# Optimization experiments

Hardware: AMD Instinct MI355X
Metric: run time of the kernel (lower is better)

## Reference

```python
import jax, jax.numpy as jnp
import numpy as np

N, E, IN_CH, C, H, L, NCLS = 4096, 131072, 512, 256, 4, 3, 2
DH = C // H  # MHA head dim


def _ln(x, g, b, eps=1e-5):
    mu = x.mean(-1, keepdims=True)
    var = ((x - mu) ** 2).mean(-1, keepdims=True)
    return (x - mu) * jax.lax.rsqrt(var + eps) * g + b


def _gelu(x):
    return jax.nn.gelu(x, approximate=False)  # torch nn.GELU default (erf)


def _gatv2(x, src, dst, wl, wr, att, b):
    # x: [N,C]; wl/wr: [H*C, C]; att: [H,C]; b: [C]
    xl = (x @ wl.T).reshape(N, H, C)  # source transform
    e = jax.nn.leaky_relu(xl[src] + (x @ wr.T).reshape(N, H, C)[dst], 0.2)  # [Et,H,C]
    score = jnp.einsum('ehc,hc->eh', e, att)  # [Et,H]
    m = jax.ops.segment_max(score, dst, num_segments=N)
    ex = jnp.exp(score - m[dst])
    denom = jax.ops.segment_sum(ex, dst, num_segments=N)
    alpha = ex / denom[dst]  # segment softmax over incoming edges
    out = jax.ops.segment_sum(alpha[:, :, None] * xl[src], dst, num_segments=N)
    return out.mean(axis=1) + b  # concat=False -> head mean


def _mha(x, in_w, in_b, out_w, out_b):
    qkv = x @ in_w.T + in_b  # [N,3C]
    q, k, v = [t.reshape(N, H, DH) for t in jnp.split(qkv, 3, axis=-1)]
    scores = jnp.einsum('nhd,mhd->hnm', q, k) / np.sqrt(DH)
    probs = jax.nn.softmax(scores, axis=-1)
    o = jnp.einsum('hnm,mhd->nhd', probs, v).reshape(N, C)
    return o @ out_w.T + out_b


def setup_inputs() -> dict:
    key = jax.random.key(0)
    ks = iter(jax.random.split(key, 64))
    s = lambda shape, sc=0.05: jax.random.normal(next(ks), shape, jnp.float32) * sc
    d = {
        'x': jax.random.normal(next(ks), (N, IN_CH), jnp.float32),
        'edge_index': jax.random.randint(next(ks), (2, E), 0, N, jnp.int32),
        'in_w': s((C, IN_CH)), 'in_b': jnp.zeros((C,), jnp.float32),
        'gat_wl': s((L, H * C, C)), 'gat_wr': s((L, H * C, C)),
        'gat_att': s((L, H, C)), 'gat_b': jnp.zeros((L, C), jnp.float32),
        'mha_in_w': s((L, 3 * C, C)), 'mha_in_b': jnp.zeros((L, 3 * C), jnp.float32),
        'mha_out_w': s((L, C, C)), 'mha_out_b': jnp.zeros((L, C), jnp.float32),
        'ln1_g': jnp.ones((L, C), jnp.float32), 'ln1_b': jnp.zeros((L, C), jnp.float32),
        'ln2_g': jnp.ones((L, C), jnp.float32), 'ln2_b': jnp.zeros((L, C), jnp.float32),
        'ln3_g': jnp.ones((L, C), jnp.float32), 'ln3_b': jnp.zeros((L, C), jnp.float32),
        'ffn_w1': s((L, 2 * C, C)), 'ffn_b1': jnp.zeros((L, 2 * C), jnp.float32),
        'ffn_w2': s((L, C, 2 * C)), 'ffn_b2': jnp.zeros((L, C), jnp.float32),
        'out_w1': s((C, C)), 'out_b1': jnp.zeros((C,), jnp.float32),
        'out_w2': s((NCLS, C)), 'out_b2': jnp.zeros((NCLS,), jnp.float32),
    }
    return d


def reference(x, edge_index, in_w, in_b, gat_wl, gat_wr, gat_att, gat_b,
              mha_in_w, mha_in_b, mha_out_w, mha_out_b,
              ln1_g, ln1_b, ln2_g, ln2_b, ln3_g, ln3_b,
              ffn_w1, ffn_b1, ffn_w2, ffn_b2,
              out_w1, out_b1, out_w2, out_b2):
    # add self loops (PyG GATv2Conv default)
    loop = jnp.arange(N, dtype=edge_index.dtype)
    src = jnp.concatenate([edge_index[0], loop])
    dst = jnp.concatenate([edge_index[1], loop])

    h = x @ in_w.T + in_b  # input_proj
    for l in range(L):
        local = _gatv2(h, src, dst, gat_wl[l], gat_wr[l], gat_att[l], gat_b[l])
        h = _ln(h + local, ln1_g[l], ln1_b[l])
        attn = _mha(h, mha_in_w[l], mha_in_b[l], mha_out_w[l], mha_out_b[l])
        h = _ln(h + attn, ln2_g[l], ln2_b[l])
        ffn = _gelu(h @ ffn_w1[l].T + ffn_b1[l]) @ ffn_w2[l].T + ffn_b2[l]
        h = _ln(h + ffn, ln3_g[l], ln3_b[l])
    h = _gelu(h @ out_w1.T + out_b1)
    return h @ out_w2.T + out_b2
```

## Files before the change

kernel.cpp:

```cpp
#include <hip/hip_runtime.h>
#include <cstdint>
#include <cstddef>

typedef unsigned short u16;
typedef __bf16 bf16x8 __attribute__((ext_vector_type(8)));
typedef float f32x4 __attribute__((ext_vector_type(4)));

constexpr int kN  = 4096;
constexpr int kE  = 131072;
constexpr int kET = kE + kN;
constexpr int kIn = 512;
constexpr int kC  = 256;
constexpr int kL  = 3;

constexpr int NSPLIT = 4;
constexpr int KSPAN  = kN / NSPLIT;
constexpr int NSTEP  = KSPAN / 64;

__device__ __forceinline__ u16 f2bf(float f) {
    unsigned u = __builtin_bit_cast(unsigned, f);
    u += 0x7fffu + ((u >> 16) & 1u);
    return (u16)(u >> 16);
}
__device__ __forceinline__ float bf2f(u16 s) {
    unsigned u = ((unsigned)s) << 16;
    return __builtin_bit_cast(float, u);
}
__device__ __forceinline__ float gelu_erf(float x) {
    return 0.5f * x * (1.f + erff(x * 0.70710678118654752f));
}
__device__ __forceinline__ void gload_lds16(const u16* gsrc, u16* ldst) {
    __builtin_amdgcn_global_load_lds(
        (const __attribute__((address_space(1))) unsigned int*)gsrc,
        (__attribute__((address_space(3))) unsigned int*)ldst, 16, 0, 0);
}
__device__ __forceinline__ float dpp_ror_add16(float x) {
    int t;
    t = __builtin_amdgcn_update_dpp(0, __builtin_bit_cast(int, x), 0x121, 0xf, 0xf, true);
    x += __builtin_bit_cast(float, t);
    t = __builtin_amdgcn_update_dpp(0, __builtin_bit_cast(int, x), 0x122, 0xf, 0xf, true);
    x += __builtin_bit_cast(float, t);
    t = __builtin_amdgcn_update_dpp(0, __builtin_bit_cast(int, x), 0x124, 0xf, 0xf, true);
    x += __builtin_bit_cast(float, t);
    t = __builtin_amdgcn_update_dpp(0, __builtin_bit_cast(int, x), 0x128, 0xf, 0xf, true);
    x += __builtin_bit_cast(float, t);
    return x;
}
__device__ __forceinline__ void unpack8(uint4 u, float* x) {
    x[0] = __builtin_bit_cast(float, u.x << 16);
    x[1] = __builtin_bit_cast(float, u.x & 0xffff0000u);
    x[2] = __builtin_bit_cast(float, u.y << 16);
    x[3] = __builtin_bit_cast(float, u.y & 0xffff0000u);
    x[4] = __builtin_bit_cast(float, u.z << 16);
    x[5] = __builtin_bit_cast(float, u.z & 0xffff0000u);
    x[6] = __builtin_bit_cast(float, u.w << 16);
    x[7] = __builtin_bit_cast(float, u.w & 0xffff0000u);
}

__global__ void cast_f2b(const float* __restrict__ src, u16* __restrict__ dst, int n4) {
    int i = blockIdx.x * blockDim.x + threadIdx.x;
    if (i >= n4) return;
    float4 v = ((const float4*)src)[i];
    ushort4 o;
    o.x = f2bf(v.x); o.y = f2bf(v.y); o.z = f2bf(v.z); o.w = f2bf(v.w);
    ((ushort4*)dst)[i] = o;
}

__global__ void csr_count(const int* __restrict__ ei, int* __restrict__ cnt) {
    int e = blockIdx.x * 256 + threadIdx.x;
    if (e >= kET) return;
    int d = (e < kE) ? ei[kE + e] : (e - kE);
    atomicAdd(cnt + d, 1);
}

__global__ __launch_bounds__(1024) void csr_scan(int* __restrict__ cnt_cur, int* __restrict__ off) {
    __shared__ int lds[1024];
    int t = threadIdx.x;
    int c[4], s = 0;
#pragma unroll
    for (int j = 0; j < 4; ++j) { c[j] = cnt_cur[t * 4 + j]; s += c[j]; }
    lds[t] = s;
    __syncthreads();
    for (int d = 1; d < 1024; d <<= 1) {
        int v = (t >= d) ? lds[t - d] : 0;
        __syncthreads();
        lds[t] += v;
        __syncthreads();
    }
    int excl = lds[t] - s;
#pragma unroll
    for (int j = 0; j < 4; ++j) { off[t * 4 + j] = excl; cnt_cur[t * 4 + j] = excl; excl += c[j]; }
    if (t == 1023) off[4096] = excl;
}

__global__ void csr_scatter(const int* __restrict__ ei, int* __restrict__ cur, int* __restrict__ csrc) {
    int e = blockIdx.x * 256 + threadIdx.x;
    if (e >= kET) return;
    int s, d;
    if (e < kE) { s = ei[e]; d = ei[kE + e]; } else { s = d = e - kE; }
    int pos = atomicAdd(cur + d, 1);
    csrc[pos] = s;
}

template <int BM, int K, int ACT, int WF32, int WBF16>
__global__ __launch_bounds__(256) void gemm_st(
    const u16* __restrict__ A, const u16* __restrict__ W,
    const float* __restrict__ bias, float* __restrict__ Cf,
    u16* __restrict__ Cb, int N) {
    constexpr int BK = 32;
    constexpr int NK = K / BK;
    constexpr int MF = BM / 32;
    int tid = threadIdx.x;
    int w = tid >> 6, lane = tid & 63;
    int wr = w >> 1, wc = w & 1;
    int g = lane >> 4, r = lane & 15;
    int bm = blockIdx.y * BM;
    int bn = blockIdx.x * 64;
    __shared__ __align__(16) u16 Ab[2][BM * BK];
    __shared__ __align__(16) u16 Bb[2][64 * BK];
    int srow = w * 16 + (lane >> 2);
    int scol = (lane & 3) * 8;
    auto stage = [&](int buf, int k0) {
#pragma unroll
        for (int i = 0; i < BM / 64; ++i)
            gload_lds16(A + (size_t)(bm + i * 64 + srow) * K + k0 + scol,
                        &Ab[buf][(i * 64 + w * 16) * BK]);
        gload_lds16(W + (size_t)(bn + srow) * K + k0 + scol, &Bb[buf][w * 16 * BK]);
    };
    f32x4 acc[MF][2] = {};
    stage(0, 0);
    __syncthreads();
    for (int st = 0; st < NK; ++st) {
        int cur = st & 1;
        if (st + 1 < NK) stage(cur ^ 1, (st + 1) * BK);
        const u16* Al = &Ab[cur][0];
        const u16* Bl = &Bb[cur][0];
        bf16x8 bf[2];
#pragma unroll
        for (int u = 0; u < 2; ++u)
            bf[u] = *(const bf16x8*)(Bl + (wc * 32 + u * 16 + r) * BK + g * 8);
#pragma unroll
        for (int t = 0; t < MF; ++t) {
            bf16x8 af = *(const bf16x8*)(Al + (wr * (BM / 2) + t * 16 + r) * BK + g * 8);
#pragma unroll
            for (int u = 0; u < 2; ++u)
                acc[t][u] = __builtin_amdgcn_mfma_f32_16x16x32_bf16(af, bf[u], acc[t][u], 0, 0, 0);
        }
        __syncthreads();
    }
    int r0 = bm + wr * (BM / 2) + g * 4;
    int c0 = bn + wc * 32 + r;
#pragma unroll
    for (int t = 0; t < MF; ++t)
#pragma unroll
        for (int u = 0; u < 2; ++u)
#pragma unroll
            for (int e = 0; e < 4; ++e) {
                int row = r0 + t * 16 + e, col = c0 + u * 16;
                float v = acc[t][u][e];
                if (bias) v += bias[col];
                if (ACT == 1) v = gelu_erf(v);
                if (WF32) Cf[(size_t)row * N + col] = v;
                if (WBF16) Cb[(size_t)row * N + col] = f2bf(v);
            }
}

__global__ __launch_bounds__(256) void ln_res(
    const float* hin, const float* add,
    const float* __restrict__ g, const float* __restrict__ b,
    float* hout, u16* __restrict__ hbf) {
    int row = blockIdx.x * 4 + (threadIdx.x >> 6);
    int lane = threadIdx.x & 63;
    const float4 x4 = *(const float4*)(hin + (size_t)row * kC + lane * 4);
    const float4 a4 = *(const float4*)(add + (size_t)row * kC + lane * 4);
    float v[4] = {x4.x + a4.x, x4.y + a4.y, x4.z + a4.z, x4.w + a4.w};
    float s = v[0] + v[1] + v[2] + v[3];
    for (int d = 1; d < 64; d <<= 1) s += __shfl_xor(s, d);
    float mu = s * (1.f / kC);
    float q = 0.f;
#pragma unroll
    for (int j = 0; j < 4; ++j) { float d = v[j] - mu; q += d * d; }
    for (int d = 1; d < 64; d <<= 1) q += __shfl_xor(q, d);
    float rstd = rsqrtf(q * (1.f / kC) + 1e-5f);
    const float4 g4 = *(const float4*)(g + lane * 4);
    const float4 b4 = *(const float4*)(b + lane * 4);
    float y0 = (v[0] - mu) * rstd * g4.x + b4.x;
    float y1 = (v[1] - mu) * rstd * g4.y + b4.y;
    float y2 = (v[2] - mu) * rstd * g4.z + b4.z;
    float y3 = (v[3] - mu) * rstd * g4.w + b4.w;
    *(float4*)(hout + (size_t)row * kC + lane * 4) = make_float4(y0, y1, y2, y3);
    ushort4 o; o.x = f2bf(y0); o.y = f2bf(y1); o.z = f2bf(y2); o.w = f2bf(y3);
    *(ushort4*)(hbf + (size_t)row * kC + lane * 4) = o;
}

__global__ __launch_bounds__(256) void gat_agg(
    const u16* __restrict__ xg,
    const float* __restrict__ att, const float* __restrict__ gb,
    const int* __restrict__ off, const int* __restrict__ srcs,
    const float* __restrict__ lng, const float* __restrict__ lnb,
    float* __restrict__ h, u16* __restrict__ hbf) {
    int n = blockIdx.x;
    int w = threadIdx.x >> 6, lane = threadIdx.x & 63;
    int q = lane >> 4, t = lane & 15;
    int cb = w * 256 + t * 16;

    uint4 xru0 = *(const uint4*)(xg + (size_t)n * 2048 + 1024 + cb);
    uint4 xru1 = *(const uint4*)(xg + (size_t)n * 2048 + 1024 + cb + 8);
    float xrv[16];
    unpack8(xru0, xrv); unpack8(xru1, xrv + 8);
    float att6[16], att4[16];
#pragma unroll
    for (int j = 0; j < 16; j += 4) {
        float4 a4 = *(const float4*)(att + cb + j);
        att6[j] = 0.6f * a4.x; att6[j + 1] = 0.6f * a4.y;
        att6[j + 2] = 0.6f * a4.z; att6[j + 3] = 0.6f * a4.w;
        att4[j] = (2.f / 3.f) * att6[j]; att4[j + 1] = (2.f / 3.f) * att6[j + 1];
        att4[j + 2] = (2.f / 3.f) * att6[j + 2]; att4[j + 3] = (2.f / 3.f) * att6[j + 3];
    }

    int i0 = off[n], i1 = off[n + 1];
    float m = -1e30f, ls = 0.f;
    float acc[16] = {};
    int i = i0 + q;
    uint4 p0a, p1a, p0b, p1b;
    if (i < i1) {
        int s = srcs[i];
        p0a = *(const uint4*)(xg + (size_t)s * 2048 + cb);
        p1a = *(const uint4*)(xg + (size_t)s * 2048 + cb + 8);
    }
    if (i + 4 < i1) {
        int s = srcs[i + 4];
        p0b = *(const uint4*)(xg + (size_t)s * 2048 + cb);
        p1b = *(const uint4*)(xg + (size_t)s * 2048 + cb + 8);
    }
    while (i < i1) {
        uint4 c0 = p0a, c1 = p1a;
        p0a = p0b; p1a = p1b;
        if (i + 8 < i1) {
            int s2 = srcs[i + 8];
            p0b = *(const uint4*)(xg + (size_t)s2 * 2048 + cb);
            p1b = *(const uint4*)(xg + (size_t)s2 * 2048 + cb + 8);
        }
        float x[16];
        unpack8(c0, x); unpack8(c1, x + 8);
        float p = 0.f;
#pragma unroll
        for (int j = 0; j < 16; ++j) {
            float e = x[j] + xrv[j];
            p = fmaf(att6[j], e, p);
            p = fmaf(att4[j], __builtin_fabsf(e), p);
        }
        p = dpp_ror_add16(p);
        if (p > m) {
            float c = __expf(m - p);
            ls = ls * c + 1.f;
#pragma unroll
            for (int j = 0; j < 16; ++j) acc[j] = acc[j] * c + x[j];
            m = p;
        } else {
            float pw = __expf(p - m);
            ls += pw;
#pragma unroll
            for (int j = 0; j < 16; ++j) acc[j] = fmaf(pw, x[j], acc[j]);
        }
        i += 4;
    }
    float mm = fmaxf(m, __shfl_xor(m, 16));
    mm = fmaxf(mm, __shfl_xor(mm, 32));
    float c = __expf(m - mm);
    ls *= c;
    ls += __shfl_xor(ls, 16);
    ls += __shfl_xor(ls, 32);
#pragma unroll
    for (int j = 0; j < 16; ++j) {
        float a = acc[j] * c;
        a += __shfl_xor(a, 16);
        a += __shfl_xor(a, 32);
        acc[j] = a;
    }
    float inv = 1.f / ls;
    __shared__ float red[4][256];
    __shared__ float rs[8];
    if (q == 0) {
#pragma unroll
        for (int j = 0; j < 16; ++j) red[w][t * 16 + j] = acc[j] * inv;
    }
    __syncthreads();
    int cc = threadIdx.x;
    float vsum = 0.25f * (red[0][cc] + red[1][cc] + red[2][cc] + red[3][cc]) + gb[cc];
    float v = h[(size_t)n * kC + cc] + vsum;
    float s1 = v, s2 = v * v;
    for (int d = 1; d < 64; d <<= 1) { s1 += __shfl_xor(s1, d); s2 += __shfl_xor(s2, d); }
    if (lane == 0) { rs[w] = s1; rs[4 + w] = s2; }
    __syncthreads();
    s1 = rs[0] + rs[1] + rs[2] + rs[3];
    s2 = rs[4] + rs[5] + rs[6] + rs[7];
    float mu = s1 * (1.f / kC);
    float rstd = rsqrtf(s2 * (1.f / kC) - mu * mu + 1e-5f);
    float y = (v - mu) * rstd * lng[cc] + lnb[cc];
    h[(size_t)n * kC + cc] = y;
    hbf[(size_t)n * kC + cc] = f2bf(y);
}

__global__ __launch_bounds__(256) void qkv_repack(
    const u16* __restrict__ qkvb, u16* __restrict__ Qb, u16* __restrict__ Kb,
    u16* __restrict__ VTb) {
    int h = blockIdx.y;
    int n0 = blockIdx.x * 64;
    int t = threadIdx.x;
    int nr = t >> 2, cb = (t & 3) * 16;
    const u16* src = qkvb + (size_t)(n0 + nr) * 768 + h * 64 + cb;
    u16* qd = Qb + ((size_t)h * kN + n0 + nr) * 64 + cb;
    u16* kd = Kb + ((size_t)h * kN + n0 + nr) * 64 + cb;
    __shared__ u16 lds[64][72];
    constexpr float QS = 0.125f * 1.4426950408889634f;
#pragma unroll
    for (int j = 0; j < 16; j += 4) {
        ushort4 q4 = *(const ushort4*)(src + j);
        ushort4 k4 = *(const ushort4*)(src + 256 + j);
        ushort4 v4 = *(const ushort4*)(src + 512 + j);
        ushort4 qo;
        qo.x = f2bf(bf2f(q4.x) * QS); qo.y = f2bf(bf2f(q4.y) * QS);
        qo.z = f2bf(bf2f(q4.z) * QS); qo.w = f2bf(bf2f(q4.w) * QS);
        *(ushort4*)(qd + j) = qo;
        *(ushort4*)(kd + j) = k4;
        *(ushort4*)(&lds[nr][cb + j]) = v4;
    }
    __syncthreads();
    int d = t >> 2, nb = (t & 3) * 16;
    u16* vd = VTb + ((size_t)h * 64 + d) * kN + n0 + nb;
#pragma unroll
    for (int j = 0; j < 16; j += 4) {
        ushort4 vo;
        vo.x = lds[nb + j + 0][d];
        vo.y = lds[nb + j + 1][d];
        vo.z = lds[nb + j + 2][d];
        vo.w = lds[nb + j + 3][d];
        *(ushort4*)(vd + j) = vo;
    }
}

__global__ __launch_bounds__(256, 4) void mha_mfma2(
    const u16* __restrict__ Qb, const u16* __restrict__ Kb,
    const u16* __restrict__ VTb, float* __restrict__ opart, float* __restrict__ mlpart) {
    int qt = blockIdx.x, head = blockIdx.y, sp = blockIdx.z;
    int tid = threadIdx.x;
    int w = tid >> 6, lane = tid & 63;
    int g = lane >> 4, r = lane & 15;
    int q0 = qt * 64;
    const u16* Qh = Qb + ((size_t)head * kN + q0 + w * 16) * 64;
    const u16* Kh = Kb + (size_t)head * kN * 64;
    const u16* VTh = VTb + (size_t)head * 64 * kN;
    __shared__ u16 Kt[2][64 * 64];
    __shared__ u16 Vt[2][64 * 64];
    __shared__ u16 plds[4][16 * 64];
    int srow = w * 8 + (lane >> 3);
    int schunk = ((lane & 7) ^ ((lane >> 3) & 7)) * 8;
    int kbase = sp * KSPAN;

    bf16x8 qf0 = *(const bf16x8*)(Qh + r * 64 + g * 8);
    bf16x8 qf1 = *(const bf16x8*)(Qh + r * 64 + 32 + g * 8);

    auto stage = [&](int buf, int k0) {
#pragma unroll
        for (int i = 0; i < 2; ++i) {
            int row = i * 32 + srow;
            gload_lds16(Kh + (size_t)(k0 + row) * 64 + schunk, &Kt[buf][(i * 32 + w * 8) * 64]);
            gload_lds16(VTh + (size_t)row * kN + k0 + schunk, &Vt[buf][(i * 32 + w * 8) * 64]);
        }
    };

    f32x4 o[4] = {};
    float m = -3.0e38f, l = 0.f;

    stage(0, kbase);
    __syncthreads();

    int rx = r & 7;
    for (int st = 0; st < NSTEP; ++st) {
        int cur = st & 1;
        if (st + 1 < NSTEP) stage(cur ^ 1, kbase + (st + 1) * 64);
        const u16* Kl = &Kt[cur][0];
        const u16* Vl = &Vt[cur][0];
        f32x4 stt[4] = {};
#pragma unroll
        for (int t = 0; t < 4; ++t) {
            bf16x8 kf0 = *(const bf16x8*)(Kl + (16 * t + r) * 64 + ((0 + g) ^ rx) * 8);
            bf16x8 kf1 = *(const bf16x8*)(Kl + (16 * t + r) * 64 + ((4 + g) ^ rx) * 8);
            stt[t] = __builtin_amdgcn_mfma_f32_16x16x32_bf16(kf0, qf0, stt[t], 0, 0, 0);
            stt[t] = __builtin_amdgcn_mfma_f32_16x16x32_bf16(kf1, qf1, stt[t], 0, 0, 0);
        }
        float pm = stt[0][0];
#pragma unroll
        for (int t = 0; t < 4; ++t)
#pragma unroll
            for (int e = 0; e < 4; ++e) pm = fmaxf(pm, stt[t][e]);
        pm = fmaxf(pm, __shfl_xor(pm, 16));
        pm = fmaxf(pm, __shfl_xor(pm, 32));
        if (__any(pm > m)) {
            float mn = fmaxf(m, pm);
            float corr = __builtin_amdgcn_exp2f(m - mn);
            l *= corr;
            float corrq[4];
#pragma unroll
            for (int e = 0; e < 4; ++e) corrq[e] = __shfl(corr, g * 4 + e);
#pragma unroll
            for (int dt = 0; dt < 4; ++dt)
#pragma unroll
                for (int e = 0; e < 4; ++e) o[dt][e] *= corrq[e];
            m = mn;
        }
        float ls = 0.f;
        float p[4][4];
#pragma unroll
        for (int t = 0; t < 4; ++t)
#pragma unroll
            for (int e = 0; e < 4; ++e) { p[t][e] = __builtin_amdgcn_exp2f(stt[t][e] - m); ls += p[t][e]; }
        ls += __shfl_xor(ls, 16);
        ls += __shfl_xor(ls, 32);
        l += ls;
#pragma unroll
        for (int t = 0; t < 4; ++t) {
            ushort4 pk;
            pk.x = f2bf(p[t][0]); pk.y = f2bf(p[t][1]);
            pk.z = f2bf(p[t][2]); pk.w = f2bf(p[t][3]);
            int lc = (2 * t + (g >> 1)) ^ rx;
            *(ushort4*)(&plds[w][r * 64 + lc * 8 + (g & 1) * 4]) = pk;
        }
        bf16x8 pa0 = *(const bf16x8*)(&plds[w][r * 64 + (g ^ rx) * 8]);
        bf16x8 pa1 = *(const bf16x8*)(&plds[w][r * 64 + ((4 + g) ^ rx) * 8]);
#pragma unroll
        for (int dt = 0; dt < 4; ++dt) {
            bf16x8 vf0 = *(const bf16x8*)(Vl + (dt * 16 + r) * 64 + ((0 + g) ^ rx) * 8);
            bf16x8 vf1 = *(const bf16x8*)(Vl + (dt * 16 + r) * 64 + ((4 + g) ^ rx) * 8);
            o[dt] = __builtin_amdgcn_mfma_f32_16x16x32_bf16(pa0, vf0, o[dt], 0, 0, 0);
            o[dt] = __builtin_amdgcn_mfma_f32_16x16x32_bf16(pa1, vf1, o[dt], 0, 0, 0);
        }
        __syncthreads();
    }

    size_t slot = (size_t)(head * 64 + qt) * NSPLIT + sp;
    float* ob = opart + slot * 4096;
#pragma unroll
    for (int dt = 0; dt < 4; ++dt)
#pragma unroll
        for (int e = 0; e < 4; ++e)
            ob[(w * 16 + g * 4 + e) * 64 + dt * 16 + r] = o[dt][e];
    float* mlb = mlpart + slot * 128;
    if (g == 0) { mlb[w * 16 + r] = m; mlb[64 + w * 16 + r] = l; }
}

__global__ __launch_bounds__(256) void mha_merge(
    const float* __restrict__ opart, const float* __restrict__ mlpart,
    u16* __restrict__ attnb) {
    int head = blockIdx.y;
    int q = blockIdx.x * 4 + (threadIdx.x >> 6);
    int d = threadIdx.x & 63;
    int qt = q >> 6, ql = q & 63;
    size_t sb = (size_t)(head * 64 + qt) * NSPLIT;
    float ms[NSPLIT], lsv[NSPLIT];
    float mstar = -3.0e38f;
#pragma unroll
    for (int s = 0; s < NSPLIT; ++s) {
        ms[s] = mlpart[(sb + s) * 128 + ql];
        lsv[s] = mlpart[(sb + s) * 128 + 64 + ql];
        mstar = fmaxf(mstar, ms[s]);
    }
    float acc = 0.f, lsum = 0.f;
#pragma unroll
    for (int s = 0; s < NSPLIT; ++s) {
        float wgt = __builtin_amdgcn_exp2f(ms[s] - mstar);
        lsum += lsv[s] * wgt;
        acc += opart[(sb + s) * 4096 + ql * 64 + d] * wgt;
    }
    attnb[(size_t)q * kC + head * 64 + d] = f2bf(acc / lsum);
}

__global__ __launch_bounds__(256) void final_out(
    const u16* __restrict__ tbf, const float* __restrict__ w2,
    const float* __restrict__ b2, float* __restrict__ out) {
    int row = blockIdx.x * 4 + (threadIdx.x >> 6);
    int lane = threadIdx.x & 63;
    const ushort4 tv = *(const ushort4*)(tbf + (size_t)row * 256 + lane * 4);
    float t0 = bf2f(tv.x), t1 = bf2f(tv.y), t2 = bf2f(tv.z), t3 = bf2f(tv.w);
    const float4 w0 = *(const float4*)(w2 + lane * 4);
    const float4 w1 = *(const float4*)(w2 + 256 + lane * 4);
    float d0 = t0 * w0.x + t1 * w0.y + t2 * w0.z + t3 * w0.w;
    float d1 = t0 * w1.x + t1 * w1.y + t2 * w1.z + t3 * w1.w;
    for (int d = 1; d < 64; d <<= 1) { d0 += __shfl_xor(d0, d); d1 += __shfl_xor(d1, d); }
    if (lane == 0) {
        out[(size_t)row * 2 + 0] = d0 + b2[0];
        out[(size_t)row * 2 + 1] = d1 + b2[1];
    }
}

extern "C" void kernel_launch(void* const* d_in, const int* in_sizes, int n_in,
                              void* d_out, int out_size, void* d_ws, size_t ws_size,
                              hipStream_t stream) {
    (void)in_sizes; (void)n_in; (void)out_size;
    const float* x        = (const float*)d_in[0];
    const int*   ei       = (const int*)d_in[1];
    const float* in_w     = (const float*)d_in[2];
    const float* in_b     = (const float*)d_in[3];
    const float* gat_wl   = (const float*)d_in[4];
    const float* gat_wr   = (const float*)d_in[5];
    const float* gat_att  = (const float*)d_in[6];
    const float* gat_b    = (const float*)d_in[7];
    const float* mha_in_w = (const float*)d_in[8];
    const float* mha_in_b = (const float*)d_in[9];
    const float* mha_out_w= (const float*)d_in[10];
    const float* mha_out_b= (const float*)d_in[11];
    const float* ln1_g = (const float*)d_in[12];
    const float* ln1_b = (const float*)d_in[13];
    const float* ln2_g = (const float*)d_in[14];
    const float* ln2_b = (const float*)d_in[15];
    const float* ln3_g = (const float*)d_in[16];
    const float* ln3_b = (const float*)d_in[17];
    const float* ffn_w1 = (const float*)d_in[18];
    const float* ffn_b1 = (const float*)d_in[19];
    const float* ffn_w2 = (const float*)d_in[20];
    const float* ffn_b2 = (const float*)d_in[21];
    const float* out_w1 = (const float*)d_in[22];
    const float* out_b1 = (const float*)d_in[23];
    const float* out_w2 = (const float*)d_in[24];
    const float* out_b2 = (const float*)d_in[25];
    float* out = (float*)d_out;

    char* ws = (char*)d_ws;
    size_t off = 0;
    auto alloc = [&](size_t bytes) -> void* {
        void* p = (void*)(ws + off);
        off += (bytes + 255) & ~(size_t)255;
        return p;
    };
    float* h     = (float*)alloc((size_t)kN * kC * 4);
    u16*   hbf   = (u16*)  alloc((size_t)kN * kC * 2);
    float* xlb   = (float*)alloc((size_t)kN * 1024 * 4);
    float* xrb   = (float*)alloc((size_t)kN * 1024 * 4);
    float* qkv   = (float*)alloc((size_t)kN * 768 * 4);
    float* locb  = (float*)alloc((size_t)kN * kC * 4);
    u16*   attnb = (u16*)  alloc((size_t)kN * kC * 2);
    u16*   midb  = (u16*)  alloc((size_t)kN * 512 * 2);
    u16*   tbf   = (u16*)  alloc((size_t)kN * kC * 2);
    u16*   xbf   = (u16*)  alloc((size_t)kN * kIn * 2);
    u16*   wbf   = (u16*)  alloc((size_t)3342336 * 2);
    int*   coff  = (int*)  alloc((size_t)4097 * 4);
    int*   ccur  = (int*)  alloc((size_t)4096 * 4);
    int*   csrc  = (int*)  alloc((size_t)kET * 4);
    if (ws_size < off) return;

    u16* xgbf = (u16*)xlb;
    u16* Qb  = (u16*)xlb;
    u16* Kb  = Qb + (size_t)4 * kN * 64;
    u16* VTb = Kb + (size_t)4 * kN * 64;
    u16* qkvb = (u16*)qkv;
    float* opart  = xrb;
    float* mlpart = locb;

    const size_t OFF_INW  = 0;
    const size_t OFF_GAT  = 131072;
    const size_t OFF_MIN  = 1703936;
    const size_t OFF_MOUT = 2293760;
    const size_t OFF_F1   = 2490368;
    const size_t OFF_F2   = 2883584;
    const size_t OFF_O1   = 3276800;

    auto cast = [&](const float* s, u16* d, int n) {
        int n4 = n >> 2;
        cast_f2b<<<dim3((n4 + 255) / 256), dim3(256), 0, stream>>>(s, d, n4);
    };
    cast(x, xbf, kN * kIn);
    cast(in_w, wbf + OFF_INW, kC * kIn);
    for (int l = 0; l < kL; ++l) {
        cast(gat_wl + (size_t)l * 262144, wbf + OFF_GAT + (size_t)l * 524288, 262144);
        cast(gat_wr + (size_t)l * 262144, wbf + OFF_GAT + (size_t)l * 524288 + 262144, 262144);
    }
    cast(mha_in_w, wbf + OFF_MIN, kL * 768 * kC);
    cast(mha_out_w, wbf + OFF_MOUT, kL * kC * kC);
    cast(ffn_w1, wbf + OFF_F1, kL * 512 * kC);
    cast(ffn_w2, wbf + OFF_F2, kL * kC * 512);
    cast(out_w1, wbf + OFF_O1, kC * kC);

    hipMemsetAsync(ccur, 0, 4096 * 4, stream);
    csr_count<<<dim3((kET + 255) / 256), dim3(256), 0, stream>>>(ei, ccur);
    csr_scan<<<dim3(1), dim3(1024), 0, stream>>>(ccur, coff);
    csr_scatter<<<dim3((kET + 255) / 256), dim3(256), 0, stream>>>(ei, ccur, csrc);

    gemm_st<64, 512, 0, 1, 1><<<dim3(kC / 64, kN / 64), dim3(256), 0, stream>>>(
        xbf, wbf + OFF_INW, in_b, h, hbf, kC);

    for (int l = 0; l < kL; ++l) {
        gemm_st<128, 256, 0, 0, 1><<<dim3(2048 / 64, kN / 128), dim3(256), 0, stream>>>(
            hbf, wbf + OFF_GAT + (size_t)l * 524288, nullptr, nullptr, xgbf, 2048);
        gat_agg<<<dim3(kN), dim3(256), 0, stream>>>(
            xgbf, gat_att + (size_t)l * 1024, gat_b + (size_t)l * kC, coff, csrc,
            ln1_g + (size_t)l * kC, ln1_b + (size_t)l * kC, h, hbf);

        gemm_st<128, 256, 0, 0, 1><<<dim3(768 / 64, kN / 128), dim3(256), 0, stream>>>(
            hbf, wbf + OFF_MIN + (size_t)l * 768 * kC, mha_in_b + (size_t)l * 768, nullptr, qkvb, 768);
        qkv_repack<<<dim3(kN / 64, 4), dim3(256), 0, stream>>>(qkvb, Qb, Kb, VTb);
        mha_mfma2<<<dim3(kN / 64, 4, NSPLIT), dim3(256), 0, stream>>>(Qb, Kb, VTb, opart, mlpart);
        mha_merge<<<dim3(kN / 4, 4), dim3(256), 0, stream>>>(opart, mlpart, attnb);
        gemm_st<64, 256, 0, 1, 0><<<dim3(kC / 64, kN / 64), dim3(256), 0, stream>>>(
            attnb, wbf + OFF_MOUT + (size_t)l * kC * kC, mha_out_b + (size_t)l * kC, locb, nullptr, kC);
        ln_res<<<dim3(kN / 4), dim3(256), 0, stream>>>(
            h, locb, ln2_g + (size_t)l * kC, ln2_b + (size_t)l * kC, h, hbf);

        gemm_st<64, 256, 1, 0, 1><<<dim3(512 / 64, kN / 64), dim3(256), 0, stream>>>(
            hbf, wbf + OFF_F1 + (size_t)l * 512 * kC, ffn_b1 + (size_t)l * 512, nullptr, midb, 512);
        gemm_st<64, 512, 0, 1, 0><<<dim3(kC / 64, kN / 64), dim3(256), 0, stream>>>(
            midb, wbf + OFF_F2 + (size_t)l * kC * 512, ffn_b2 + (size_t)l * kC, locb, nullptr, kC);
        ln_res<<<dim3(kN / 4), dim3(256), 0, stream>>>(
            h, locb, ln3_g + (size_t)l * kC, ln3_b + (size_t)l * kC, h, hbf);
    }

    gemm_st<64, 256, 1, 0, 1><<<dim3(kC / 64, kN / 64), dim3(256), 0, stream>>>(
        hbf, wbf + OFF_O1, out_b1, nullptr, tbf, kC);
    final_out<<<dim3(kN / 4), dim3(256), 0, stream>>>(tbf, out_w2, out_b2, out);
}
```

Before: 529.0 us.

## Fuse residual LayerNorm into output GEMMs and add 128x128 tile GAT projection GEMM

```diff
diff --git a/kernel.cpp b/kernel.cpp
--- a/kernel.cpp
+++ b/kernel.cpp
@@ -165,32 +165,154 @@
             }
 }
 
-__global__ __launch_bounds__(256) void ln_res(
-    const float* hin, const float* add,
-    const float* __restrict__ g, const float* __restrict__ b,
-    float* hout, u16* __restrict__ hbf) {
-    int row = blockIdx.x * 4 + (threadIdx.x >> 6);
-    int lane = threadIdx.x & 63;
-    const float4 x4 = *(const float4*)(hin + (size_t)row * kC + lane * 4);
-    const float4 a4 = *(const float4*)(add + (size_t)row * kC + lane * 4);
-    float v[4] = {x4.x + a4.x, x4.y + a4.y, x4.z + a4.z, x4.w + a4.w};
-    float s = v[0] + v[1] + v[2] + v[3];
-    for (int d = 1; d < 64; d <<= 1) s += __shfl_xor(s, d);
-    float mu = s * (1.f / kC);
-    float q = 0.f;
-#pragma unroll
-    for (int j = 0; j < 4; ++j) { float d = v[j] - mu; q += d * d; }
-    for (int d = 1; d < 64; d <<= 1) q += __shfl_xor(q, d);
-    float rstd = rsqrtf(q * (1.f / kC) + 1e-5f);
-    const float4 g4 = *(const float4*)(g + lane * 4);
-    const float4 b4 = *(const float4*)(b + lane * 4);
-    float y0 = (v[0] - mu) * rstd * g4.x + b4.x;
-    float y1 = (v[1] - mu) * rstd * g4.y + b4.y;
-    float y2 = (v[2] - mu) * rstd * g4.z + b4.z;
-    float y3 = (v[3] - mu) * rstd * g4.w + b4.w;
-    *(float4*)(hout + (size_t)row * kC + lane * 4) = make_float4(y0, y1, y2, y3);
-    ushort4 o; o.x = f2bf(y0); o.y = f2bf(y1); o.z = f2bf(y2); o.w = f2bf(y3);
-    *(ushort4*)(hbf + (size_t)row * kC + lane * 4) = o;
+template <int K>
+__global__ __launch_bounds__(256) void gemm_128(
+    const u16* __restrict__ A, const u16* __restrict__ W,
+    u16* __restrict__ Cb, int N) {
+    constexpr int BK = 32;
+    constexpr int NK = K / BK;
+    int tid = threadIdx.x;
+    int w = tid >> 6, lane = tid & 63;
+    int wr = w >> 1, wc = w & 1;
+    int g = lane >> 4, r = lane & 15;
+    int bm = blockIdx.y * 128;
+    int bn = blockIdx.x * 128;
+    __shared__ __align__(16) u16 Ab[2][128 * BK];
+    __shared__ __align__(16) u16 Bb[2][128 * BK];
+    int srd = lane >> 2;
+    int schunk = ((lane & 3) ^ ((lane >> 3) & 3)) * 8;
+    auto stage = [&](int buf, int k0) {
+#pragma unroll
+        for (int i = 0; i < 2; ++i) {
+            int rowA = bm + i * 64 + w * 16 + srd;
+            int rowB = bn + i * 64 + w * 16 + srd;
+            gload_lds16(A + (size_t)rowA * K + k0 + schunk, &Ab[buf][(i * 64 + w * 16) * BK]);
+            gload_lds16(W + (size_t)rowB * K + k0 + schunk, &Bb[buf][(i * 64 + w * 16) * BK]);
+        }
+    };
+    f32x4 acc[4][4] = {};
+    stage(0, 0);
+    __syncthreads();
+    int rs = (r >> 1) & 3;
+    for (int st = 0; st < NK; ++st) {
+        int cur = st & 1;
+        if (st + 1 < NK) stage(cur ^ 1, (st + 1) * BK);
+        const u16* Al = &Ab[cur][0];
+        const u16* Bl = &Bb[cur][0];
+        bf16x8 bf[4];
+#pragma unroll
+        for (int u = 0; u < 4; ++u)
+            bf[u] = *(const bf16x8*)(Bl + (wc * 64 + u * 16 + r) * BK + ((g ^ rs) * 8));
+#pragma unroll
+        for (int t = 0; t < 4; ++t) {
+            bf16x8 af = *(const bf16x8*)(Al + (wr * 64 + t * 16 + r) * BK + ((g ^ rs) * 8));
+#pragma unroll
+            for (int u = 0; u < 4; ++u)
+                acc[t][u] = __builtin_amdgcn_mfma_f32_16x16x32_bf16(af, bf[u], acc[t][u], 0, 0, 0);
+        }
+        __syncthreads();
+    }
+#pragma unroll
+    for (int t = 0; t < 4; ++t)
+#pragma unroll
+        for (int u = 0; u < 4; ++u)
+#pragma unroll
+            for (int e = 0; e < 4; ++e) {
+                int row = bm + wr * 64 + t * 16 + g * 4 + e;
+                int col = bn + wc * 64 + u * 16 + r;
+                Cb[(size_t)row * N + col] = f2bf(acc[t][u][e]);
+            }
+}
+
+template <int K>
+__global__ __launch_bounds__(256) void gemm_ln(
+    const u16* __restrict__ A, const u16* __restrict__ W,
+    const float* __restrict__ bias,
+    const float* __restrict__ lng, const float* __restrict__ lnb,
+    float* __restrict__ h, u16* __restrict__ hbf) {
+    constexpr int BK = 32;
+    constexpr int NK = K / BK;
+    int tid = threadIdx.x;
+    int w = tid >> 6, lane = tid & 63;
+    int g = lane >> 4, r = lane & 15;
+    int bm = blockIdx.x * 32;
+    __shared__ __align__(16) u16 Ab[2][32 * BK];
+    __shared__ __align__(16) u16 Bb[2][256 * BK];
+    __shared__ float sums[32][4][2];
+    int srd = lane >> 2;
+    int schunk = ((lane & 3) ^ ((lane >> 3) & 3)) * 8;
+    auto stage = [&](int buf, int k0) {
+        if (w < 2)
+            gload_lds16(A + (size_t)(bm + w * 16 + srd) * K + k0 + schunk,
+                        &Ab[buf][(w * 16) * BK]);
+#pragma unroll
+        for (int i = 0; i < 4; ++i)
+            gload_lds16(W + (size_t)(w * 64 + i * 16 + srd) * K + k0 + schunk,
+                        &Bb[buf][(w * 64 + i * 16) * BK]);
+    };
+    f32x4 acc[2][4] = {};
+    stage(0, 0);
+    __syncthreads();
+    int rs = (r >> 1) & 3;
+    for (int st = 0; st < NK; ++st) {
+        int cur = st & 1;
+        if (st + 1 < NK) stage(cur ^ 1, (st + 1) * BK);
+        const u16* Al = &Ab[cur][0];
+        const u16* Bl = &Bb[cur][0];
+        bf16x8 bf[4];
+#pragma unroll
+        for (int u = 0; u < 4; ++u)
+            bf[u] = *(const bf16x8*)(Bl + (w * 64 + u * 16 + r) * BK + ((g ^ rs) * 8));
+#pragma unroll
+        for (int t = 0; t < 2; ++t) {
+            bf16x8 af = *(const bf16x8*)(Al + (t * 16 + r) * BK + ((g ^ rs) * 8));
+#pragma unroll
+            for (int u = 0; u < 4; ++u)
+                acc[t][u] = __builtin_amdgcn_mfma_f32_16x16x32_bf16(af, bf[u], acc[t][u], 0, 0, 0);
+        }
+        __syncthreads();
+    }
+    float val[2][4][4];
+#pragma unroll
+    for (int t = 0; t < 2; ++t)
+#pragma unroll
+        for (int e = 0; e < 4; ++e) {
+            int row = bm + t * 16 + g * 4 + e;
+            float s1 = 0.f, s2 = 0.f;
+#pragma unroll
+            for (int u = 0; u < 4; ++u) {
+                int col = w * 64 + u * 16 + r;
+                float v = acc[t][u][e] + bias[col] + h[(size_t)row * kC + col];
+                val[t][u][e] = v;
+                s1 += v;
+                s2 += v * v;
+            }
+            s1 = dpp_ror_add16(s1);
+            s2 = dpp_ror_add16(s2);
+            if (r == 0) {
+                sums[t * 16 + g * 4 + e][w][0] = s1;
+                sums[t * 16 + g * 4 + e][w][1] = s2;
+            }
+        }
+    __syncthreads();
+#pragma unroll
+    for (int t = 0; t < 2; ++t)
+#pragma unroll
+        for (int e = 0; e < 4; ++e) {
+            int lr = t * 16 + g * 4 + e;
+            int row = bm + lr;
+            float S1 = sums[lr][0][0] + sums[lr][1][0] + sums[lr][2][0] + sums[lr][3][0];
+            float S2 = sums[lr][0][1] + sums[lr][1][1] + sums[lr][2][1] + sums[lr][3][1];
+            float mu = S1 * (1.f / kC);
+            float rstd = rsqrtf(S2 * (1.f / kC) - mu * mu + 1e-5f);
+#pragma unroll
+            for (int u = 0; u < 4; ++u) {
+                int col = w * 64 + u * 16 + r;
+                float y = (val[t][u][e] - mu) * rstd * lng[col] + lnb[col];
+                h[(size_t)row * kC + col] = y;
+                hbf[(size_t)row * kC + col] = f2bf(y);
+            }
+        }
 }
 
 __global__ __launch_bounds__(256) void gat_agg(
@@ -590,8 +712,8 @@
         xbf, wbf + OFF_INW, in_b, h, hbf, kC);
 
     for (int l = 0; l < kL; ++l) {
-        gemm_st<128, 256, 0, 0, 1><<<dim3(2048 / 64, kN / 128), dim3(256), 0, stream>>>(
-            hbf, wbf + OFF_GAT + (size_t)l * 524288, nullptr, nullptr, xgbf, 2048);
+        gemm_128<256><<<dim3(2048 / 128, kN / 128), dim3(256), 0, stream>>>(
+            hbf, wbf + OFF_GAT + (size_t)l * 524288, xgbf, 2048);
         gat_agg<<<dim3(kN), dim3(256), 0, stream>>>(
             xgbf, gat_att + (size_t)l * 1024, gat_b + (size_t)l * kC, coff, csrc,
             ln1_g + (size_t)l * kC, ln1_b + (size_t)l * kC, h, hbf);
@@ -601,17 +723,15 @@
         qkv_repack<<<dim3(kN / 64, 4), dim3(256), 0, stream>>>(qkvb, Qb, Kb, VTb);
         mha_mfma2<<<dim3(kN / 64, 4, NSPLIT), dim3(256), 0, stream>>>(Qb, Kb, VTb, opart, mlpart);
         mha_merge<<<dim3(kN / 4, 4), dim3(256), 0, stream>>>(opart, mlpart, attnb);
-        gemm_st<64, 256, 0, 1, 0><<<dim3(kC / 64, kN / 64), dim3(256), 0, stream>>>(
-            attnb, wbf + OFF_MOUT + (size_t)l * kC * kC, mha_out_b + (size_t)l * kC, locb, nullptr, kC);
-        ln_res<<<dim3(kN / 4), dim3(256), 0, stream>>>(
-            h, locb, ln2_g + (size_t)l * kC, ln2_b + (size_t)l * kC, h, hbf);
+        gemm_ln<256><<<dim3(kN / 32), dim3(256), 0, stream>>>(
+            attnb, wbf + OFF_MOUT + (size_t)l * kC * kC, mha_out_b + (size_t)l * kC,
+            ln2_g + (size_t)l * kC, ln2_b + (size_t)l * kC, h, hbf);
 
         gemm_st<64, 256, 1, 0, 1><<<dim3(512 / 64, kN / 64), dim3(256), 0, stream>>>(
             hbf, wbf + OFF_F1 + (size_t)l * 512 * kC, ffn_b1 + (size_t)l * 512, nullptr, midb, 512);
-        gemm_st<64, 512, 0, 1, 0><<<dim3(kC / 64, kN / 64), dim3(256), 0, stream>>>(
-            midb, wbf + OFF_F2 + (size_t)l * kC * 512, ffn_b2 + (size_t)l * kC, locb, nullptr, kC);
-        ln_res<<<dim3(kN / 4), dim3(256), 0, stream>>>(
-            h, locb, ln3_g + (size_t)l * kC, ln3_b + (size_t)l * kC, h, hbf);
+        gemm_ln<512><<<dim3(kN / 32), dim3(256), 0, stream>>>(
+            midb, wbf + OFF_F2 + (size_t)l * kC * 512, ffn_b2 + (size_t)l * kC,
+            ln3_g + (size_t)l * kC, ln3_b + (size_t)l * kC, h, hbf);
     }
 
     gemm_st<64, 256, 1, 0, 1><<<dim3(kC / 64, kN / 64), dim3(256), 0, stream>>>(
```

Result: no change. 522.3 us (-1.3%).
